# Kernel optimization log

Hardware: AMD Instinct MI355X
Metric: run time of the kernel (lower is better)

## Reference

```python
import jax, jax.numpy as jnp
import numpy as np

N = 50000
E = 600000
OB_DIM = 128
H = 128
P_OUT = 8


def _glorot(key, fan_in, fan_out):
    lim = float(np.sqrt(6.0 / (fan_in + fan_out)))
    return jax.random.uniform(key, (fan_in, fan_out), jnp.float32, -lim, lim)


def setup_inputs() -> dict:
    key = jax.random.key(0)
    ks = jax.random.split(key, 16)
    x = jax.random.normal(ks[0], (N, OB_DIM), jnp.float32)
    edge_index = jax.random.randint(ks[1], (2, E), 0, N, jnp.int64)
    dims = [(OB_DIM, H), (H, H), (H, P_OUT), (OB_DIM, H), (H, H), (H, 1)]
    names = ["p1", "p2", "p3", "v1", "v2", "v3"]
    inp = {"x": x, "edge_index": edge_index}
    for i, (nm, (fi, fo)) in enumerate(zip(names, dims)):
        inp["W" + nm] = _glorot(ks[2 + i], fi, fo)
        inp["b" + nm] = jnp.zeros((fo,), jnp.float32)
    return inp


def _gcn_norm(edge_index, n):
    # add self-loops, symmetric normalization deg^{-1/2} A_hat deg^{-1/2}
    loops = jnp.arange(n, dtype=edge_index.dtype)
    src = jnp.concatenate([edge_index[0], loops])
    dst = jnp.concatenate([edge_index[1], loops])
    deg = jax.ops.segment_sum(jnp.ones_like(dst, jnp.float32), dst, num_segments=n)
    dinv = jax.lax.rsqrt(jnp.maximum(deg, 1.0))
    norm = dinv[src] * dinv[dst]  # [E+N]
    return src, dst, norm


def _gcn_conv(x, W, b, src, dst, norm, n):
    h = x @ W                      # [N, out]
    msg = h[src] * norm[:, None]   # gather + scale, [E+N, out]
    out = jax.ops.segment_sum(msg, dst, num_segments=n)
    return out + b


def reference(x, edge_index, Wp1, bp1, Wp2, bp2, Wp3, bp3, Wv1, bv1, Wv2, bv2, Wv3, bv3):
    n = x.shape[0]
    src, dst, norm = _gcn_norm(edge_index, n)
    # policy branch
    a = jax.nn.relu(_gcn_conv(x, Wp1, bp1, src, dst, norm, n))
    a = jax.nn.relu(_gcn_conv(a, Wp2, bp2, src, dst, norm, n))
    action_logits = _gcn_conv(a, Wp3, bp3, src, dst, norm, n)  # Categorical logits
    # value branch
    v = jax.nn.relu(_gcn_conv(x, Wv1, bv1, src, dst, norm, n))
    v = jax.nn.relu(_gcn_conv(v, Wv2, bv2, src, dst, norm, n))
    v = _gcn_conv(v, Wv3, bv3, src, dst, norm, n)
    return action_logits, v
```

## Files before the change

### kernel.cpp

```cpp
#include <hip/hip_runtime.h>

#define NN 50000
#define NE 600000

typedef unsigned short ushort_t;
typedef ushort_t ushortx8 __attribute__((ext_vector_type(8)));
typedef ushort_t ushortx4 __attribute__((ext_vector_type(4)));
typedef short bf16x8 __attribute__((ext_vector_type(8)));
typedef float f32x4 __attribute__((ext_vector_type(4)));
typedef int intx2 __attribute__((ext_vector_type(2)));
typedef float fltx4 __attribute__((ext_vector_type(4)));

__device__ __forceinline__ float bf2f(ushort_t u) {
    union { unsigned int i; float f; } c;
    c.i = ((unsigned int)u) << 16;
    return c.f;
}
__device__ __forceinline__ ushort_t f2bf(float f) {
    union { float f; unsigned int i; } c;
    c.f = f;
    unsigned int u = c.i;
    unsigned int r = u + 0x7FFFu + ((u >> 16) & 1u);
    return (ushort_t)(r >> 16);
}
__device__ __forceinline__ unsigned cvtpk(float lo, float hi) {
    unsigned r;
    asm("v_cvt_pk_bf16_f32 %0, %1, %2" : "=v"(r) : "v"(lo), "v"(hi));
    return r;
}


__global__ void k_count(const int* __restrict__ ei, int* __restrict__ cnt) {
    int e = blockIdx.x * 256 + threadIdx.x;
    if (e < NE) {
        int d = __builtin_nontemporal_load(ei + NE + e);
        atomicAdd(&cnt[d], 1);
    }
}

__global__ void k_scan1(const int* __restrict__ cnt, int* __restrict__ rowptr,
                        int* __restrict__ bsum, float* __restrict__ dinv) {
    __shared__ int s[256];
    int t = threadIdx.x;
    int i = blockIdx.x * 256 + t;
    int v = (i < NN) ? cnt[i] : 0;
    if (i < NN) dinv[i] = rsqrtf(1.0f + (float)v);
    s[t] = v;
    __syncthreads();
    for (int d = 1; d < 256; d <<= 1) {
        int tmp = (t >= d) ? s[t - d] : 0;
        __syncthreads();
        s[t] += tmp;
        __syncthreads();
    }
    if (i < NN) rowptr[i] = s[t] - v;
    if (t == 255) bsum[blockIdx.x] = s[255];
}

__global__ void k_scan2_prep(int* __restrict__ bsum, int* __restrict__ boff, int nb,
                             const float* __restrict__ Wp1, const float* __restrict__ Wv1,
                             const float* __restrict__ Wp2, const float* __restrict__ Wv2,
                             ushort_t* __restrict__ Wt1, ushort_t* __restrict__ Wt2p,
                             ushort_t* __restrict__ Wt2v) {
    int b = blockIdx.x, t = threadIdx.x;
    if (b < 128) {
        int idx = b * 256 + t;
        int n = idx >> 7, k = idx & 127;
        float v = (n < 128) ? Wp1[k * 128 + n] : Wv1[k * 128 + (n - 128)];
        Wt1[n * 128 + k] = f2bf(v);
    } else if (b < 192) {
        int idx = (b - 128) * 256 + t;
        int n = idx >> 7, k = idx & 127;
        Wt2p[n * 128 + k] = f2bf(Wp2[k * 128 + n]);
    } else if (b < 256) {
        int idx = (b - 192) * 256 + t;
        int n = idx >> 7, k = idx & 127;
        Wt2v[n * 128 + k] = f2bf(Wv2[k * 128 + n]);
    } else {
        __shared__ int s[256];
        int v = (t < nb) ? bsum[t] : 0;
        s[t] = v;
        __syncthreads();
        for (int d = 1; d < 256; d <<= 1) {
            int tmp = (t >= d) ? s[t - d] : 0;
            __syncthreads();
            s[t] += tmp;
            __syncthreads();
        }
        boff[t] = s[t] - v;
    }
}

__global__ void k_scan3rc(const int* __restrict__ rowptr, const int* __restrict__ cnt,
                          const int* __restrict__ boff, int2* __restrict__ rc) {
    int i = blockIdx.x * 256 + threadIdx.x;
    if (i < NN) {
        int2 v;
        v.x = rowptr[i] + boff[blockIdx.x];
        v.y = cnt[i];
        rc[i] = v;
    }
}

__global__ void k_fill(const int* __restrict__ ei, const int2* __restrict__ rc,
                       int* __restrict__ fill, const float* __restrict__ dinv,
                       int2* __restrict__ edges) {
    int e = blockIdx.x * 256 + threadIdx.x;
    if (e < NE) {
        int s = __builtin_nontemporal_load(ei + e);
        int d = __builtin_nontemporal_load(ei + NE + e);
        int pos = rc[d].x + atomicAdd(&fill[d], 1);
        int2 pr;
        pr.x = s;
        pr.y = __float_as_int(dinv[s] * dinv[d]);
        edges[pos] = pr;
    }
}

__global__ __launch_bounds__(256) void k_gemm1(const float* __restrict__ X,
                                               const ushort_t* __restrict__ Wt1,
                                               ushort_t* __restrict__ C, int nrows) {
    __shared__ ushort_t Wl[256 * 128];
    int t = threadIdx.x;
    const ushortx8* Wg = (const ushortx8*)Wt1;
#pragma unroll
    for (int i = 0; i < 16; ++i) {
        int c = i * 256 + t;
        int row = c >> 4, slot = c & 15;
        int db = row * 256 + ((slot * 16) ^ ((row & 7) << 4));
        *(ushortx8*)((char*)Wl + db) = Wg[c];
    }
    __syncthreads();

    int w = t >> 6, l = t & 63, m = l & 15, g = l >> 4;
    int r0 = blockIdx.x * 64 + w * 16;
    if (r0 >= nrows) return;

    const float* Arow = X + (size_t)(r0 + m) * 128;
    bf16x8 af[4];
#pragma unroll
    for (int kk = 0; kk < 4; ++kk) {
        float4 lo = *(const float4*)(Arow + kk * 32 + g * 8);
        float4 hi = *(const float4*)(Arow + kk * 32 + g * 8 + 4);
        union { unsigned u[4]; bf16x8 v; } cv;
        cv.u[0] = cvtpk(lo.x, lo.y);
        cv.u[1] = cvtpk(lo.z, lo.w);
        cv.u[2] = cvtpk(hi.x, hi.y);
        cv.u[3] = cvtpk(hi.z, hi.w);
        af[kk] = cv.v;
    }

    f32x4 acc[16];
#pragma unroll
    for (int nt = 0; nt < 16; ++nt) acc[nt] = (f32x4){0.f, 0.f, 0.f, 0.f};
    int sw = (m & 7) << 4;
#pragma unroll
    for (int nt = 0; nt < 16; ++nt) {
        const char* Wb = (const char*)Wl + (nt * 16 + m) * 256;
#pragma unroll
        for (int kk = 0; kk < 4; ++kk) {
            bf16x8 wf = *(const bf16x8*)(Wb + ((kk * 64 + g * 16) ^ sw));
            acc[nt] = __builtin_amdgcn_mfma_f32_16x16x32_bf16(wf, af[kk], acc[nt], 0, 0, 0);
        }
    }
#pragma unroll
    for (int nt = 0; nt < 16; ++nt) {
        ushortx4 o = {f2bf(acc[nt][0]), f2bf(acc[nt][1]), f2bf(acc[nt][2]), f2bf(acc[nt][3])};
        *(ushortx4*)(C + (size_t)(r0 + m) * 256 + nt * 16 + g * 4) = o;
    }
}

__global__ __launch_bounds__(256) void k_gemm2(const ushort_t* __restrict__ A,
                                               const ushort_t* __restrict__ Wp,
                                               const ushort_t* __restrict__ Wv,
                                               ushort_t* __restrict__ C, int nrows) {
    __shared__ ushort_t Wl[2 * 128 * 128];
    int t = threadIdx.x;
    const ushortx8* Wgp = (const ushortx8*)Wp;
    const ushortx8* Wgv = (const ushortx8*)Wv;
#pragma unroll
    for (int i = 0; i < 8; ++i) {
        int c = i * 256 + t;
        int row = c >> 4, slot = c & 15;
        int db = row * 256 + ((slot * 16) ^ ((row & 7) << 4));
        *(ushortx8*)((char*)Wl + db) = Wgp[c];
        *(ushortx8*)((char*)Wl + 32768 + db) = Wgv[c];
    }
    __syncthreads();

    int w = t >> 6, l = t & 63, m = l & 15, g = l >> 4;
    int r0 = blockIdx.x * 64 + w * 16;
    if (r0 >= nrows) return;

    const ushort_t* Arow = A + (size_t)(r0 + m) * 256;
    bf16x8 alo[4], ahi[4];
#pragma unroll
    for (int kk = 0; kk < 4; ++kk) {
        alo[kk] = *(const bf16x8*)(Arow + kk * 32 + g * 8);
        ahi[kk] = *(const bf16x8*)(Arow + 128 + kk * 32 + g * 8);
    }

    f32x4 accp[8], accv[8];
#pragma unroll
    for (int nt = 0; nt < 8; ++nt) {
        accp[nt] = (f32x4){0.f, 0.f, 0.f, 0.f};
        accv[nt] = (f32x4){0.f, 0.f, 0.f, 0.f};
    }
    int sw = (m & 7) << 4;
#pragma unroll
    for (int nt = 0; nt < 8; ++nt) {
        const char* Wbp = (const char*)Wl + (nt * 16 + m) * 256;
        const char* Wbv = Wbp + 32768;
#pragma unroll
        for (int kk = 0; kk < 4; ++kk) {
            int off = (kk * 64 + g * 16) ^ sw;
            bf16x8 wfp = *(const bf16x8*)(Wbp + off);
            accp[nt] = __builtin_amdgcn_mfma_f32_16x16x32_bf16(wfp, alo[kk], accp[nt], 0, 0, 0);
            bf16x8 wfv = *(const bf16x8*)(Wbv + off);
            accv[nt] = __builtin_amdgcn_mfma_f32_16x16x32_bf16(wfv, ahi[kk], accv[nt], 0, 0, 0);
        }
    }
#pragma unroll
    for (int nt = 0; nt < 8; ++nt) {
        ushortx4 op = {f2bf(accp[nt][0]), f2bf(accp[nt][1]), f2bf(accp[nt][2]), f2bf(accp[nt][3])};
        ushortx4 ov = {f2bf(accv[nt][0]), f2bf(accv[nt][1]), f2bf(accv[nt][2]), f2bf(accv[nt][3])};
        *(ushortx4*)(C + (size_t)(r0 + m) * 256 + nt * 16 + g * 4) = op;
        *(ushortx4*)(C + (size_t)(r0 + m) * 256 + 128 + nt * 16 + g * 4) = ov;
    }
}

__global__ __launch_bounds__(256) void k_agg256(const ushort_t* __restrict__ H,
                                                ushort_t* __restrict__ OUT,
                                                const float* __restrict__ b_lo,
                                                const float* __restrict__ b_hi,
                                                const float* __restrict__ dinv,
                                                const int2* __restrict__ rc,
                                                const int2* __restrict__ edges) {
    int wv = threadIdx.x >> 6;
    int l = threadIdx.x & 63;
    int i = blockIdx.x * 4 + wv;
    if (i >= NN) return;
    int h = l >> 5, q = l & 31;
    const ushortx8* H8 = (const ushortx8*)H;

    float a0[8] = {}, a1[8] = {};
    float di = dinv[i];
    float ws = (h == 0) ? di * di : 0.f;
    ushortx8 hv = H8[(size_t)i * 32 + q];
#pragma unroll
    for (int k = 0; k < 8; ++k) a0[k] = ws * bf2f(hv[k]);

    int2 rcv = rc[i];
    int st = rcv.x, n = rcv.y;

    for (int j = h; j < n; j += 8) {
        int idx[4];
        float w[4];
#pragma unroll
        for (int s = 0; s < 4; ++s) {
            int jj = j + 2 * s;
            bool valid = jj < n;
            intx2 em = __builtin_nontemporal_load(
                (const intx2*)edges + (valid ? st + jj : st));
            idx[s] = valid ? em.x : i;
            w[s] = valid ? __int_as_float(em.y) : 0.f;
        }
        ushortx8 hh[4];
#pragma unroll
        for (int s = 0; s < 4; ++s) hh[s] = H8[(size_t)idx[s] * 32 + q];
#pragma unroll
        for (int k = 0; k < 8; ++k) a0[k] += w[0] * bf2f(hh[0][k]);
#pragma unroll
        for (int k = 0; k < 8; ++k) a1[k] += w[1] * bf2f(hh[1][k]);
#pragma unroll
        for (int k = 0; k < 8; ++k) a0[k] += w[2] * bf2f(hh[2][k]);
#pragma unroll
        for (int k = 0; k < 8; ++k) a1[k] += w[3] * bf2f(hh[3][k]);
    }
#pragma unroll
    for (int k = 0; k < 8; ++k) a0[k] += a1[k];
#pragma unroll
    for (int k = 0; k < 8; ++k) a0[k] += __shfl_xor(a0[k], 32, 64);

    if (h == 0) {
        const float* bb = (q < 16) ? (b_lo + q * 8) : (b_hi + (q - 16) * 8);
        float4 b0 = *(const float4*)bb;
        float4 b1 = *(const float4*)(bb + 4);
        float r[8];
        r[0] = fmaxf(a0[0] + b0.x, 0.f); r[1] = fmaxf(a0[1] + b0.y, 0.f);
        r[2] = fmaxf(a0[2] + b0.z, 0.f); r[3] = fmaxf(a0[3] + b0.w, 0.f);
        r[4] = fmaxf(a0[4] + b1.x, 0.f); r[5] = fmaxf(a0[5] + b1.y, 0.f);
        r[6] = fmaxf(a0[6] + b1.z, 0.f); r[7] = fmaxf(a0[7] + b1.w, 0.f);
        ushortx8 o = {f2bf(r[0]), f2bf(r[1]), f2bf(r[2]), f2bf(r[3]),
                      f2bf(r[4]), f2bf(r[5]), f2bf(r[6]), f2bf(r[7])};
        __builtin_nontemporal_store(o, (ushortx8*)OUT + (size_t)i * 32 + q);
    }
}

__global__ __launch_bounds__(256) void k_small(const ushort_t* __restrict__ F2,
                                               const float* __restrict__ Wp3,
                                               const float* __restrict__ Wv3,
                                               float* __restrict__ FS) {
    __shared__ float Wp[8 * 128];
    __shared__ float Wv[128];
    int t = threadIdx.x;
    for (int j = t; j < 1024; j += 256) {
        int k = j >> 3, c = j & 7;
        Wp[c * 128 + k] = Wp3[j];
    }
    if (t < 128) Wv[t] = Wv3[t];
    __syncthreads();
    int row = blockIdx.x * 256 + t;
    if (row >= NN) return;
    const ushortx8* F8 = (const ushortx8*)F2;
    size_t base = (size_t)row * 32;
    float acc[9] = {};
#pragma unroll 2
    for (int kc = 0; kc < 16; ++kc) {
        ushortx8 p = F8[base + kc];
        ushortx8 v = F8[base + 16 + kc];
#pragma unroll
        for (int jj = 0; jj < 8; ++jj) {
            float pv = bf2f(p[jj]);
            int k = kc * 8 + jj;
#pragma unroll
            for (int c = 0; c < 8; ++c) acc[c] += pv * Wp[c * 128 + k];
            acc[8] += bf2f(v[jj]) * Wv[k];
        }
    }
    float4* FSo = (float4*)(FS + (size_t)row * 12);
    float4 o0 = {acc[0], acc[1], acc[2], acc[3]};
    float4 o1 = {acc[4], acc[5], acc[6], acc[7]};
    float4 o2 = {acc[8], 0.f, 0.f, 0.f};
    FSo[0] = o0; FSo[1] = o1; FSo[2] = o2;
}

__global__ void k_agg9(const float* __restrict__ FS, float* __restrict__ out_logits,
                       float* __restrict__ out_v, const float* __restrict__ bp3,
                       const float* __restrict__ bv3, const float* __restrict__ dinv,
                       const int2* __restrict__ rc, const int2* __restrict__ edges) {
    int i = blockIdx.x * 256 + threadIdx.x;
    if (i >= NN) return;
    float di = dinv[i];
    float w0 = di * di;
    const float4* F = (const float4*)FS;
    size_t b0 = (size_t)i * 3;
    float4 x0 = F[b0], x1 = F[b0 + 1], x2 = F[b0 + 2];
    float a[9];
    a[0] = w0 * x0.x; a[1] = w0 * x0.y; a[2] = w0 * x0.z; a[3] = w0 * x0.w;
    a[4] = w0 * x1.x; a[5] = w0 * x1.y; a[6] = w0 * x1.z; a[7] = w0 * x1.w;
    a[8] = w0 * x2.x;
    int2 rcv = rc[i];
    int st = rcv.x, n = rcv.y;
    for (int j = 0; j < n; ++j) {
        int2 e = edges[st + j];
        float w = __int_as_float(e.y);
        size_t sb = (size_t)e.x * 3;
        float4 y0 = F[sb], y1 = F[sb + 1], y2 = F[sb + 2];
        a[0] += w * y0.x; a[1] += w * y0.y; a[2] += w * y0.z; a[3] += w * y0.w;
        a[4] += w * y1.x; a[5] += w * y1.y; a[6] += w * y1.z; a[7] += w * y1.w;
        a[8] += w * y2.x;
    }
    float4 bpa = *(const float4*)bp3;
    float4 bpb = *(const float4*)(bp3 + 4);
    fltx4 o0 = {a[0] + bpa.x, a[1] + bpa.y, a[2] + bpa.z, a[3] + bpa.w};
    fltx4 o1 = {a[4] + bpb.x, a[5] + bpb.y, a[6] + bpb.z, a[7] + bpb.w};
    __builtin_nontemporal_store(o0, (fltx4*)out_logits + (size_t)i * 2);
    __builtin_nontemporal_store(o1, (fltx4*)out_logits + (size_t)i * 2 + 1);
    __builtin_nontemporal_store(a[8] + bv3[0], out_v + i);
}

extern "C" void kernel_launch(void* const* d_in, const int* in_sizes, int n_in,
                              void* d_out, int out_size, void* d_ws, size_t ws_size,
                              hipStream_t stream) {
    const float* x   = (const float*)d_in[0];
    const int*   ei  = (const int*)d_in[1];
    const float* Wp1 = (const float*)d_in[2],  *bp1 = (const float*)d_in[3];
    const float* Wp2 = (const float*)d_in[4],  *bp2 = (const float*)d_in[5];
    const float* Wp3 = (const float*)d_in[6],  *bp3 = (const float*)d_in[7];
    const float* Wv1 = (const float*)d_in[8],  *bv1 = (const float*)d_in[9];
    const float* Wv2 = (const float*)d_in[10], *bv2 = (const float*)d_in[11];
    const float* Wv3 = (const float*)d_in[12], *bv3 = (const float*)d_in[13];
    float* out_logits = (float*)d_out;
    float* out_v = (float*)d_out + (size_t)NN * 8;

    char* w = (char*)d_ws;
    auto alloc = [&](size_t bytes) {
        char* p = w;
        w += (bytes + 255) & ~(size_t)255;
        return p;
    };
    int*      cntfill = (int*)alloc((size_t)2 * NN * 4);
    int*      cnt    = cntfill;
    int*      fill   = cntfill + NN;
    int*      rowptr = (int*)alloc(NN * 4);
    int*      bsum   = (int*)alloc(256 * 4);
    int*      boff   = (int*)alloc(256 * 4);
    float*    dinv   = (float*)alloc(NN * 4);
    int2*     rc     = (int2*)alloc((size_t)NN * 8);
    int2*     edges  = (int2*)alloc((size_t)NE * 8);
    ushort_t* Wt1    = (ushort_t*)alloc(256 * 128 * 2);
    ushort_t* Wt2p   = (ushort_t*)alloc(128 * 128 * 2);
    ushort_t* Wt2v   = (ushort_t*)alloc(128 * 128 * 2);
    ushort_t* Hb     = (ushort_t*)alloc((size_t)NN * 256 * 2);
    ushort_t* f1b    = (ushort_t*)alloc((size_t)NN * 256 * 2);
    ushort_t* f2b    = (ushort_t*)alloc((size_t)NN * 256 * 2);
    float*    fs     = (float*)alloc((size_t)NN * 12 * 4);

    const int NB = (NN + 255) / 256;
    const int EB = (NE + 255) / 256;
    const int GB = (NN + 63) / 64;
    const int AB = NN / 4;

    (void)hipMemsetAsync(cntfill, 0, (size_t)2 * NN * 4, stream);
    k_count<<<EB, 256, 0, stream>>>(ei, cnt);
    k_scan1<<<NB, 256, 0, stream>>>(cnt, rowptr, bsum, dinv);
    k_scan2_prep<<<257, 256, 0, stream>>>(bsum, boff, NB, Wp1, Wv1, Wp2, Wv2,
                                          Wt1, Wt2p, Wt2v);
    k_scan3rc<<<NB, 256, 0, stream>>>(rowptr, cnt, boff, rc);
    k_fill<<<EB, 256, 0, stream>>>(ei, rc, fill, dinv, edges);

    k_gemm1<<<GB, 256, 0, stream>>>(x, Wt1, Hb, NN);
    k_agg256<<<AB, 256, 0, stream>>>(Hb, f1b, bp1, bv1, dinv, rc, edges);
    k_gemm2<<<GB, 256, 0, stream>>>(f1b, Wt2p, Wt2v, Hb, NN);
    k_agg256<<<AB, 256, 0, stream>>>(Hb, f2b, bp2, bv2, dinv, rc, edges);
    k_small<<<NB, 256, 0, stream>>>(f2b, Wp3, Wv3, fs);
    k_agg9<<<NB, 256, 0, stream>>>(fs, out_logits, out_v, bp3, bv3, dinv, rc, edges);
}
```

Measured before the change: 237.6 us.

## Aggregate before transform in first layer using shared 128-wide input aggregation

Reorders the layers as (A X) W instead of A (X W). The first layer now aggregates the 128-wide bf16 input once for both branches rather than the 256-wide concatenated projection, so that gather touches half the bytes. Bias and ReLU move into the GEMM epilogues, and a separate kernel converts x to bf16 up front. The cost is an extra conversion kernel and pass over x, plus more intermediate buffers. Rounding order changes slightly because aggregation now happens in bf16 before the matmul.

Result: faster. 219.3 us (-7.7%).

```diff
diff --git a/kernel.cpp b/kernel.cpp
--- a/kernel.cpp
+++ b/kernel.cpp
@@ -27,6 +27,18 @@
     unsigned r;
     asm("v_cvt_pk_bf16_f32 %0, %1, %2" : "=v"(r) : "v"(lo), "v"(hi));
     return r;
+}
+
+__global__ void k_xbf(const float* __restrict__ X, ushort_t* __restrict__ XB) {
+    size_t i = (size_t)blockIdx.x * 256 + threadIdx.x;
+    const float4* X4 = (const float4*)X;
+    float4 a = X4[i * 2], b = X4[i * 2 + 1];
+    union { unsigned u[4]; ushortx8 v; } cv;
+    cv.u[0] = cvtpk(a.x, a.y);
+    cv.u[1] = cvtpk(a.z, a.w);
+    cv.u[2] = cvtpk(b.x, b.y);
+    cv.u[3] = cvtpk(b.z, b.w);
+    __builtin_nontemporal_store(cv.v, (ushortx8*)XB + i);
 }
 
 
@@ -117,122 +129,68 @@
     }
 }
 
-__global__ __launch_bounds__(256) void k_gemm1(const float* __restrict__ X,
-                                               const ushort_t* __restrict__ Wt1,
-                                               ushort_t* __restrict__ C, int nrows) {
-    __shared__ ushort_t Wl[256 * 128];
-    int t = threadIdx.x;
-    const ushortx8* Wg = (const ushortx8*)Wt1;
-#pragma unroll
-    for (int i = 0; i < 16; ++i) {
-        int c = i * 256 + t;
-        int row = c >> 4, slot = c & 15;
-        int db = row * 256 + ((slot * 16) ^ ((row & 7) << 4));
-        *(ushortx8*)((char*)Wl + db) = Wg[c];
-    }
-    __syncthreads();
-
-    int w = t >> 6, l = t & 63, m = l & 15, g = l >> 4;
-    int r0 = blockIdx.x * 64 + w * 16;
-    if (r0 >= nrows) return;
-
-    const float* Arow = X + (size_t)(r0 + m) * 128;
-    bf16x8 af[4];
-#pragma unroll
-    for (int kk = 0; kk < 4; ++kk) {
-        float4 lo = *(const float4*)(Arow + kk * 32 + g * 8);
-        float4 hi = *(const float4*)(Arow + kk * 32 + g * 8 + 4);
-        union { unsigned u[4]; bf16x8 v; } cv;
-        cv.u[0] = cvtpk(lo.x, lo.y);
-        cv.u[1] = cvtpk(lo.z, lo.w);
-        cv.u[2] = cvtpk(hi.x, hi.y);
-        cv.u[3] = cvtpk(hi.z, hi.w);
-        af[kk] = cv.v;
-    }
-
-    f32x4 acc[16];
-#pragma unroll
-    for (int nt = 0; nt < 16; ++nt) acc[nt] = (f32x4){0.f, 0.f, 0.f, 0.f};
-    int sw = (m & 7) << 4;
-#pragma unroll
-    for (int nt = 0; nt < 16; ++nt) {
-        const char* Wb = (const char*)Wl + (nt * 16 + m) * 256;
-#pragma unroll
-        for (int kk = 0; kk < 4; ++kk) {
-            bf16x8 wf = *(const bf16x8*)(Wb + ((kk * 64 + g * 16) ^ sw));
-            acc[nt] = __builtin_amdgcn_mfma_f32_16x16x32_bf16(wf, af[kk], acc[nt], 0, 0, 0);
+__global__ __launch_bounds__(256) void k_agg128(const ushort_t* __restrict__ H,
+                                                ushort_t* __restrict__ OUT,
+                                                const float* __restrict__ dinv,
+                                                const int2* __restrict__ rc,
+                                                const int2* __restrict__ edges) {
+    int wv = threadIdx.x >> 6;
+    int l = threadIdx.x & 63;
+    int i = blockIdx.x * 4 + wv;
+    if (i >= NN) return;
+    int t2 = l >> 4, q = l & 15;
+    const ushortx8* H8 = (const ushortx8*)H;
+
+    float a0[8] = {}, a1[8] = {};
+    float di = dinv[i];
+    float ws = (t2 == 0) ? di * di : 0.f;
+    ushortx8 hv = H8[(size_t)i * 16 + q];
+#pragma unroll
+    for (int k = 0; k < 8; ++k) a0[k] = ws * bf2f(hv[k]);
+
+    int2 rcv = rc[i];
+    int st = rcv.x, n = rcv.y;
+
+    for (int j = t2; j < n; j += 16) {
+        int idx[4];
+        float w[4];
+#pragma unroll
+        for (int s = 0; s < 4; ++s) {
+            int jj = j + 4 * s;
+            bool valid = jj < n;
+            intx2 em = __builtin_nontemporal_load(
+                (const intx2*)edges + (valid ? st + jj : st));
+            idx[s] = valid ? em.x : i;
+            w[s] = valid ? __int_as_float(em.y) : 0.f;
         }
-    }
-#pragma unroll
-    for (int nt = 0; nt < 16; ++nt) {
-        ushortx4 o = {f2bf(acc[nt][0]), f2bf(acc[nt][1]), f2bf(acc[nt][2]), f2bf(acc[nt][3])};
-        *(ushortx4*)(C + (size_t)(r0 + m) * 256 + nt * 16 + g * 4) = o;
-    }
-}
-
-__global__ __launch_bounds__(256) void k_gemm2(const ushort_t* __restrict__ A,
-                                               const ushort_t* __restrict__ Wp,
-                                               const ushort_t* __restrict__ Wv,
-                                               ushort_t* __restrict__ C, int nrows) {
-    __shared__ ushort_t Wl[2 * 128 * 128];
-    int t = threadIdx.x;
-    const ushortx8* Wgp = (const ushortx8*)Wp;
-    const ushortx8* Wgv = (const ushortx8*)Wv;
-#pragma unroll
-    for (int i = 0; i < 8; ++i) {
-        int c = i * 256 + t;
-        int row = c >> 4, slot = c & 15;
-        int db = row * 256 + ((slot * 16) ^ ((row & 7) << 4));
-        *(ushortx8*)((char*)Wl + db) = Wgp[c];
-        *(ushortx8*)((char*)Wl + 32768 + db) = Wgv[c];
-    }
-    __syncthreads();
-
-    int w = t >> 6, l = t & 63, m = l & 15, g = l >> 4;
-    int r0 = blockIdx.x * 64 + w * 16;
-    if (r0 >= nrows) return;
-
-    const ushort_t* Arow = A + (size_t)(r0 + m) * 256;
-    bf16x8 alo[4], ahi[4];
-#pragma unroll
-    for (int kk = 0; kk < 4; ++kk) {
-        alo[kk] = *(const bf16x8*)(Arow + kk * 32 + g * 8);
-        ahi[kk] = *(const bf16x8*)(Arow + 128 + kk * 32 + g * 8);
-    }
-
-    f32x4 accp[8], accv[8];
-#pragma unroll
-    for (int nt = 0; nt < 8; ++nt) {
-        accp[nt] = (f32x4){0.f, 0.f, 0.f, 0.f};
-        accv[nt] = (f32x4){0.f, 0.f, 0.f, 0.f};
-    }
-    int sw = (m & 7) << 4;
-#pragma unroll
-    for (int nt = 0; nt < 8; ++nt) {
-        const char* Wbp = (const char*)Wl + (nt * 16 + m) * 256;
-        const char* Wbv = Wbp + 32768;
-#pragma unroll
-        for (int kk = 0; kk < 4; ++kk) {
-            int off = (kk * 64 + g * 16) ^ sw;
-            bf16x8 wfp = *(const bf16x8*)(Wbp + off);
-            accp[nt] = __builtin_amdgcn_mfma_f32_16x16x32_bf16(wfp, alo[kk], accp[nt], 0, 0, 0);
-            bf16x8 wfv = *(const bf16x8*)(Wbv + off);
-            accv[nt] = __builtin_amdgcn_mfma_f32_16x16x32_bf16(wfv, ahi[kk], accv[nt], 0, 0, 0);
-        }
-    }
-#pragma unroll
-    for (int nt = 0; nt < 8; ++nt) {
-        ushortx4 op = {f2bf(accp[nt][0]), f2bf(accp[nt][1]), f2bf(accp[nt][2]), f2bf(accp[nt][3])};
-        ushortx4 ov = {f2bf(accv[nt][0]), f2bf(accv[nt][1]), f2bf(accv[nt][2]), f2bf(accv[nt][3])};
-        *(ushortx4*)(C + (size_t)(r0 + m) * 256 + nt * 16 + g * 4) = op;
-        *(ushortx4*)(C + (size_t)(r0 + m) * 256 + 128 + nt * 16 + g * 4) = ov;
+        ushortx8 hh[4];
+#pragma unroll
+        for (int s = 0; s < 4; ++s) hh[s] = H8[(size_t)idx[s] * 16 + q];
+#pragma unroll
+        for (int k = 0; k < 8; ++k) a0[k] += w[0] * bf2f(hh[0][k]);
+#pragma unroll
+        for (int k = 0; k < 8; ++k) a1[k] += w[1] * bf2f(hh[1][k]);
+#pragma unroll
+        for (int k = 0; k < 8; ++k) a0[k] += w[2] * bf2f(hh[2][k]);
+#pragma unroll
+        for (int k = 0; k < 8; ++k) a1[k] += w[3] * bf2f(hh[3][k]);
+    }
+#pragma unroll
+    for (int k = 0; k < 8; ++k) a0[k] += a1[k];
+#pragma unroll
+    for (int k = 0; k < 8; ++k) {
+        a0[k] += __shfl_xor(a0[k], 16, 64);
+        a0[k] += __shfl_xor(a0[k], 32, 64);
+    }
+    if (l < 16) {
+        ushortx8 o = {f2bf(a0[0]), f2bf(a0[1]), f2bf(a0[2]), f2bf(a0[3]),
+                      f2bf(a0[4]), f2bf(a0[5]), f2bf(a0[6]), f2bf(a0[7])};
+        __builtin_nontemporal_store(o, (ushortx8*)OUT + (size_t)i * 16 + q);
     }
 }
 
 __global__ __launch_bounds__(256) void k_agg256(const ushort_t* __restrict__ H,
                                                 ushort_t* __restrict__ OUT,
-                                                const float* __restrict__ b_lo,
-                                                const float* __restrict__ b_hi,
                                                 const float* __restrict__ dinv,
                                                 const int2* __restrict__ rc,
                                                 const int2* __restrict__ edges) {
@@ -283,17 +241,129 @@
     for (int k = 0; k < 8; ++k) a0[k] += __shfl_xor(a0[k], 32, 64);
 
     if (h == 0) {
-        const float* bb = (q < 16) ? (b_lo + q * 8) : (b_hi + (q - 16) * 8);
-        float4 b0 = *(const float4*)bb;
-        float4 b1 = *(const float4*)(bb + 4);
-        float r[8];
-        r[0] = fmaxf(a0[0] + b0.x, 0.f); r[1] = fmaxf(a0[1] + b0.y, 0.f);
-        r[2] = fmaxf(a0[2] + b0.z, 0.f); r[3] = fmaxf(a0[3] + b0.w, 0.f);
-        r[4] = fmaxf(a0[4] + b1.x, 0.f); r[5] = fmaxf(a0[5] + b1.y, 0.f);
-        r[6] = fmaxf(a0[6] + b1.z, 0.f); r[7] = fmaxf(a0[7] + b1.w, 0.f);
-        ushortx8 o = {f2bf(r[0]), f2bf(r[1]), f2bf(r[2]), f2bf(r[3]),
-                      f2bf(r[4]), f2bf(r[5]), f2bf(r[6]), f2bf(r[7])};
+        ushortx8 o = {f2bf(a0[0]), f2bf(a0[1]), f2bf(a0[2]), f2bf(a0[3]),
+                      f2bf(a0[4]), f2bf(a0[5]), f2bf(a0[6]), f2bf(a0[7])};
         __builtin_nontemporal_store(o, (ushortx8*)OUT + (size_t)i * 32 + q);
+    }
+}
+
+__global__ __launch_bounds__(256) void k_gemm1(const ushort_t* __restrict__ A,
+                                               const ushort_t* __restrict__ Wt1,
+                                               const float* __restrict__ bL,
+                                               const float* __restrict__ bH,
+                                               ushort_t* __restrict__ C, int nrows) {
+    __shared__ ushort_t Wl[256 * 128];
+    int t = threadIdx.x;
+    const ushortx8* Wg = (const ushortx8*)Wt1;
+#pragma unroll
+    for (int i = 0; i < 16; ++i) {
+        int c = i * 256 + t;
+        int row = c >> 4, slot = c & 15;
+        int db = row * 256 + ((slot * 16) ^ ((row & 7) << 4));
+        *(ushortx8*)((char*)Wl + db) = Wg[c];
+    }
+    __syncthreads();
+
+    int w = t >> 6, l = t & 63, m = l & 15, g = l >> 4;
+    int r0 = blockIdx.x * 64 + w * 16;
+    if (r0 >= nrows) return;
+
+    const ushort_t* Arow = A + (size_t)(r0 + m) * 128;
+    bf16x8 af[4];
+#pragma unroll
+    for (int kk = 0; kk < 4; ++kk) af[kk] = *(const bf16x8*)(Arow + kk * 32 + g * 8);
+
+    f32x4 acc[16];
+#pragma unroll
+    for (int nt = 0; nt < 16; ++nt) acc[nt] = (f32x4){0.f, 0.f, 0.f, 0.f};
+    int sw = (m & 7) << 4;
+#pragma unroll
+    for (int nt = 0; nt < 16; ++nt) {
+        const char* Wb = (const char*)Wl + (nt * 16 + m) * 256;
+#pragma unroll
+        for (int kk = 0; kk < 4; ++kk) {
+            bf16x8 wf = *(const bf16x8*)(Wb + ((kk * 64 + g * 16) ^ sw));
+            acc[nt] = __builtin_amdgcn_mfma_f32_16x16x32_bf16(wf, af[kk], acc[nt], 0, 0, 0);
+        }
+    }
+#pragma unroll
+    for (int nt = 0; nt < 16; ++nt) {
+        const float* bb = (nt < 8) ? (bL + nt * 16 + g * 4) : (bH + (nt - 8) * 16 + g * 4);
+        float4 bv = *(const float4*)bb;
+        ushortx4 o = {f2bf(fmaxf(acc[nt][0] + bv.x, 0.f)),
+                      f2bf(fmaxf(acc[nt][1] + bv.y, 0.f)),
+                      f2bf(fmaxf(acc[nt][2] + bv.z, 0.f)),
+                      f2bf(fmaxf(acc[nt][3] + bv.w, 0.f))};
+        *(ushortx4*)(C + (size_t)(r0 + m) * 256 + nt * 16 + g * 4) = o;
+    }
+}
+
+__global__ __launch_bounds__(256) void k_gemm2(const ushort_t* __restrict__ A,
+                                               const ushort_t* __restrict__ Wp,
+                                               const ushort_t* __restrict__ Wv,
+                                               const float* __restrict__ bL,
+                                               const float* __restrict__ bH,
+                                               ushort_t* __restrict__ C, int nrows) {
+    __shared__ ushort_t Wl[2 * 128 * 128];
+    int t = threadIdx.x;
+    const ushortx8* Wgp = (const ushortx8*)Wp;
+    const ushortx8* Wgv = (const ushortx8*)Wv;
+#pragma unroll
+    for (int i = 0; i < 8; ++i) {
+        int c = i * 256 + t;
+        int row = c >> 4, slot = c & 15;
+        int db = row * 256 + ((slot * 16) ^ ((row & 7) << 4));
+        *(ushortx8*)((char*)Wl + db) = Wgp[c];
+        *(ushortx8*)((char*)Wl + 32768 + db) = Wgv[c];
+    }
+    __syncthreads();
+
+    int w = t >> 6, l = t & 63, m = l & 15, g = l >> 4;
+    int r0 = blockIdx.x * 64 + w * 16;
+    if (r0 >= nrows) return;
+
+    const ushort_t* Arow = A + (size_t)(r0 + m) * 256;
+    bf16x8 alo[4], ahi[4];
+#pragma unroll
+    for (int kk = 0; kk < 4; ++kk) {
+        alo[kk] = *(const bf16x8*)(Arow + kk * 32 + g * 8);
+        ahi[kk] = *(const bf16x8*)(Arow + 128 + kk * 32 + g * 8);
+    }
+
+    f32x4 accp[8], accv[8];
+#pragma unroll
+    for (int nt = 0; nt < 8; ++nt) {
+        accp[nt] = (f32x4){0.f, 0.f, 0.f, 0.f};
+        accv[nt] = (f32x4){0.f, 0.f, 0.f, 0.f};
+    }
+    int sw = (m & 7) << 4;
+#pragma unroll
+    for (int nt = 0; nt < 8; ++nt) {
+        const char* Wbp = (const char*)Wl + (nt * 16 + m) * 256;
+        const char* Wbv = Wbp + 32768;
+#pragma unroll
+        for (int kk = 0; kk < 4; ++kk) {
+            int off = (kk * 64 + g * 16) ^ sw;
+            bf16x8 wfp = *(const bf16x8*)(Wbp + off);
+            accp[nt] = __builtin_amdgcn_mfma_f32_16x16x32_bf16(wfp, alo[kk], accp[nt], 0, 0, 0);
+            bf16x8 wfv = *(const bf16x8*)(Wbv + off);
+            accv[nt] = __builtin_amdgcn_mfma_f32_16x16x32_bf16(wfv, ahi[kk], accv[nt], 0, 0, 0);
+        }
+    }
+#pragma unroll
+    for (int nt = 0; nt < 8; ++nt) {
+        float4 bp = *(const float4*)(bL + nt * 16 + g * 4);
+        float4 bv = *(const float4*)(bH + nt * 16 + g * 4);
+        ushortx4 op = {f2bf(fmaxf(accp[nt][0] + bp.x, 0.f)),
+                       f2bf(fmaxf(accp[nt][1] + bp.y, 0.f)),
+                       f2bf(fmaxf(accp[nt][2] + bp.z, 0.f)),
+                       f2bf(fmaxf(accp[nt][3] + bp.w, 0.f))};
+        ushortx4 ov = {f2bf(fmaxf(accv[nt][0] + bv.x, 0.f)),
+                       f2bf(fmaxf(accv[nt][1] + bv.y, 0.f)),
+                       f2bf(fmaxf(accv[nt][2] + bv.z, 0.f)),
+                       f2bf(fmaxf(accv[nt][3] + bv.w, 0.f))};
+        *(ushortx4*)(C + (size_t)(r0 + m) * 256 + nt * 16 + g * 4) = op;
+        *(ushortx4*)(C + (size_t)(r0 + m) * 256 + 128 + nt * 16 + g * 4) = ov;
     }
 }
 
@@ -402,8 +472,10 @@
     ushort_t* Wt1    = (ushort_t*)alloc(256 * 128 * 2);
     ushort_t* Wt2p   = (ushort_t*)alloc(128 * 128 * 2);
     ushort_t* Wt2v   = (ushort_t*)alloc(128 * 128 * 2);
-    ushort_t* Hb     = (ushort_t*)alloc((size_t)NN * 256 * 2);
+    ushort_t* xb     = (ushort_t*)alloc((size_t)NN * 128 * 2);
+    ushort_t* ag0    = (ushort_t*)alloc((size_t)NN * 128 * 2);
     ushort_t* f1b    = (ushort_t*)alloc((size_t)NN * 256 * 2);
+    ushort_t* ag1    = (ushort_t*)alloc((size_t)NN * 256 * 2);
     ushort_t* f2b    = (ushort_t*)alloc((size_t)NN * 256 * 2);
     float*    fs     = (float*)alloc((size_t)NN * 12 * 4);
 
@@ -412,6 +484,7 @@
     const int GB = (NN + 63) / 64;
     const int AB = NN / 4;
 
+    k_xbf<<<3125, 256, 0, stream>>>(x, xb);
     (void)hipMemsetAsync(cntfill, 0, (size_t)2 * NN * 4, stream);
     k_count<<<EB, 256, 0, stream>>>(ei, cnt);
     k_scan1<<<NB, 256, 0, stream>>>(cnt, rowptr, bsum, dinv);
@@ -420,10 +493,10 @@
     k_scan3rc<<<NB, 256, 0, stream>>>(rowptr, cnt, boff, rc);
     k_fill<<<EB, 256, 0, stream>>>(ei, rc, fill, dinv, edges);
 
-    k_gemm1<<<GB, 256, 0, stream>>>(x, Wt1, Hb, NN);
-    k_agg256<<<AB, 256, 0, stream>>>(Hb, f1b, bp1, bv1, dinv, rc, edges);
-    k_gemm2<<<GB, 256, 0, stream>>>(f1b, Wt2p, Wt2v, Hb, NN);
-    k_agg256<<<AB, 256, 0, stream>>>(Hb, f2b, bp2, bv2, dinv, rc, edges);
+    k_agg128<<<AB, 256, 0, stream>>>(xb, ag0, dinv, rc, edges);
+    k_gemm1<<<GB, 256, 0, stream>>>(ag0, Wt1, bp1, bv1, f1b, NN);
+    k_agg256<<<AB, 256, 0, stream>>>(f1b, ag1, dinv, rc, edges);
+    k_gemm2<<<GB, 256, 0, stream>>>(ag1, Wt2p, Wt2v, bp2, bv2, f2b, NN);
     k_small<<<NB, 256, 0, stream>>>(f2b, Wp3, Wv3, fs);
     k_agg9<<<NB, 256, 0, stream>>>(fs, out_logits, out_v, bp3, bv3, dinv, rc, edges);
 }
```
